# Kernel tuning notes

Measured on AMD Instinct MI355X. Metric: run time of the kernel, lower is better.

The kernel has to match this reference:

```python
import jax, jax.numpy as jnp
import numpy as np

V = 28   # len(string.ascii_lowercase + ' #')
D = 32   # embed dim
H = 2    # heads
DH = D // H
B = 64
S = 1024


def _pe(seq_len, d):
    pos = np.arange(seq_len, dtype=np.float32)[:, None]
    div = np.exp(np.arange(0, d, 2, dtype=np.float32) * (-np.log(10000.0) / d))
    pe = np.zeros((seq_len, d), np.float32)
    pe[:, 0::2] = np.sin(pos * div)
    pe[:, 1::2] = np.cos(pos * div)
    return jnp.asarray(pe)


def setup_inputs() -> dict:
    key = jax.random.key(0)
    ks = jax.random.split(key, 12)
    x = jax.random.randint(ks[0], (B, S), 0, V)
    # per-row valid length in [1, S-4] so last 1-index + 3 stays in range (as original assumes)
    lengths = jax.random.randint(ks[1], (B,), 1, S - 3)
    mask = (jnp.arange(S)[None, :] < lengths[:, None]).astype(jnp.float32)[..., None]
    sc = 1.0 / np.sqrt(D)
    emb = jax.random.normal(ks[2], (V, D), jnp.float32)
    wq = jax.random.normal(ks[3], (D, D), jnp.float32) * sc
    wk = jax.random.normal(ks[4], (D, D), jnp.float32) * sc
    wv = jax.random.normal(ks[5], (D, D), jnp.float32) * sc
    bq = jnp.zeros((D,), jnp.float32)
    bk = jnp.zeros((D,), jnp.float32)
    bv = jnp.zeros((D,), jnp.float32)
    wo = jax.random.normal(ks[6], (D, D), jnp.float32) * sc
    bo = jnp.zeros((D,), jnp.float32)
    w_fc = jax.random.normal(ks[7], (V, D), jnp.float32) * sc
    b_fc = jnp.zeros((V,), jnp.float32)
    pe = _pe(S, D)
    return {"x": x, "mask": mask, "emb": emb, "pe": pe,
            "wq": wq, "bq": bq, "wk": wk, "bk": bk, "wv": wv, "bv": bv,
            "wo": wo, "bo": bo, "w_fc": w_fc, "b_fc": b_fc}


def reference(x, mask, emb, pe, wq, bq, wk, bk, wv, bv, wo, bo, w_fc, b_fc):
    Bn, Sn = x.shape
    h = emb[x] + pe[:Sn]                      # [B,S,D]
    m = mask[..., 0]                          # [B,S]
    # vectorized "last valid index" (replaces per-row python loop + .item())
    valid = m > 0
    last = Sn - 1 - jnp.argmax(valid[:, ::-1], axis=1)   # [B]
    pos = jnp.arange(Sn)
    ext = (pos[None, :] > last[:, None]) & (pos[None, :] <= last[:, None] + 3) \
          & (last[:, None] < Sn - 1)
    nm = jnp.where(ext, jnp.float32(1.0), m)  # extended mask [B,S]
    h = h * nm[..., None]
    # multihead self-attention (torch MultiheadAttention, batch_first)
    def heads(t):
        return t.reshape(Bn, Sn, H, DH).transpose(0, 2, 1, 3)  # [B,H,S,DH]
    q = heads(h @ wq.T + bq)
    k = heads(h @ wk.T + bk)
    v = heads(h @ wv.T + bv)
    scores = jnp.einsum('bhqd,bhkd->bhqk', q, k) / jnp.sqrt(jnp.float32(DH))
    scores = jnp.where((nm == 0)[:, None, None, :], jnp.float32(-1e9), scores)
    a = jax.nn.softmax(scores, axis=-1)
    o = jnp.einsum('bhqk,bhkd->bhqd', a, v).transpose(0, 2, 1, 3).reshape(Bn, Sn, D)
    o = o @ wo.T + bo
    return o @ w_fc.T + b_fc                  # [B,S,V]
```

## Files before the change

### kernel.cpp

```cpp
#include <hip/hip_runtime.h>
#include <math.h>

#define BB 64
#define SS 1024
#define DD 32
#define HH 2
#define DHH 16
#define VV 28
#define QSC 0.3606737602222409f

typedef __attribute__((ext_vector_type(8))) short bf16x8;
typedef __attribute__((ext_vector_type(4))) float f32x4;

__device__ __forceinline__ unsigned pack_hi2(float a, float b) {
    return __builtin_amdgcn_perm(__float_as_uint(b), __float_as_uint(a), 0x07060302u);
}
__device__ __forceinline__ float trunc_hi(float a) {
    return __uint_as_float(__float_as_uint(a) & 0xFFFF0000u);
}
__device__ __forceinline__ unsigned bf_rtne_u(float x) {
    unsigned u = __float_as_uint(x);
    return (u + 0x7FFFu + ((u >> 16) & 1u)) >> 16;
}
__device__ __forceinline__ unsigned pack_rtne2(float a, float b) {
    return bf_rtne_u(a) | (bf_rtne_u(b) << 16);
}
__device__ __forceinline__ bf16x8 as_bf16x8(uint4 u) {
    union { uint4 u; bf16x8 v; } cv; cv.u = u; return cv.v;
}


__global__ __launch_bounds__(256) void k_pre(
        const int* __restrict__ x, const float* __restrict__ mask,
        const float* __restrict__ emb, const float* __restrict__ pe,
        const float* __restrict__ wq, const float* __restrict__ bq,
        const float* __restrict__ wk, const float* __restrict__ bk,
        const float* __restrict__ wv, const float* __restrict__ bv,
        const float* __restrict__ wo, const float* __restrict__ bo,
        const float* __restrict__ wfc, const float* __restrict__ bfc,
        int* __restrict__ e, float* __restrict__ W2, float* __restrict__ b2,
        char* __restrict__ qf, char* __restrict__ kf, char* __restrict__ vf) {
    int bid = blockIdx.x;
    int tid = threadIdx.x;
    if (bid < 1024) {
        __shared__ __align__(16) char hbuf[10240];
        __shared__ __align__(16) float Cb[4][16 * 17];
        char* hHi = hbuf;
        char* hLo = hbuf + 5120;
        int wave = tid >> 6, lane = tid & 63;
        int c = lane & 15, kq = lane >> 4;
        {
            int tt = tid >> 2, q4 = tid & 3;
            int idx = bid * 64 + tt;
            int b = idx >> 10, s = idx & 1023;
            float nm = (mask[b * SS + (s >= 3 ? s - 3 : 0)] != 0.0f) ? 1.0f : 0.0f;
            int tok = x[idx];
            float h[8];
#pragma unroll
            for (int i = 0; i < 8; i++)
                h[i] = (emb[tok * DD + q4 * 8 + i] + pe[s * DD + q4 * 8 + i]) * nm;
            unsigned wh[4], wl[4];
#pragma unroll
            for (int wd = 0; wd < 4; wd++) {
                float a0 = h[2 * wd], a1 = h[2 * wd + 1];
                wh[wd] = pack_hi2(a0, a1);
                wl[wd] = pack_hi2(a0 - trunc_hi(a0), a1 - trunc_hi(a1));
            }
            *(uint4*)(hHi + tt * 80 + q4 * 16) = uint4{wh[0], wh[1], wh[2], wh[3]};
            *(uint4*)(hLo + tt * 80 + q4 * 16) = uint4{wl[0], wl[1], wl[2], wl[3]};
        }
        __syncthreads();
        bf16x8 aHh, aHl;
        {
            int off = (wave * 16 + c) * 80 + kq * 16;
            aHh = *(const bf16x8*)(hHi + off);
            aHl = *(const bf16x8*)(hLo + off);
        }
        int blk_b = bid >> 4;
        int s_w = ((bid * 64) & 1023) + wave * 16;
        const f32x4 z4 = {0.0f, 0.0f, 0.0f, 0.0f};
#pragma unroll
        for (int M = 0; M < 3; M++) {
            const float* W    = M == 0 ? wq : (M == 1 ? wk : wv);
            const float* bias = M == 0 ? bq : (M == 1 ? bk : bv);
            bf16x8 Bh[2], Bl[2];
            float bv_[2];
#pragma unroll
            for (int nt = 0; nt < 2; nt++) {
                const float* wrow = W + (nt * 16 + c) * DD + kq * 8;
                float4 wa = ((const float4*)wrow)[0];
                float4 wb = ((const float4*)wrow)[1];
                float f[8] = {wa.x, wa.y, wa.z, wa.w, wb.x, wb.y, wb.z, wb.w};
                unsigned uh[4], ul[4];
#pragma unroll
                for (int wd = 0; wd < 4; wd++) {
                    float a0 = f[2 * wd], a1 = f[2 * wd + 1];
                    uh[wd] = pack_hi2(a0, a1);
                    ul[wd] = pack_hi2(a0 - trunc_hi(a0), a1 - trunc_hi(a1));
                }
                Bh[nt] = as_bf16x8(uint4{uh[0], uh[1], uh[2], uh[3]});
                Bl[nt] = as_bf16x8(uint4{ul[0], ul[1], ul[2], ul[3]});
                bv_[nt] = bias[nt * 16 + c];
            }
#pragma unroll
            for (int nt = 0; nt < 2; nt++) {
                f32x4 acc = __builtin_amdgcn_mfma_f32_16x16x32_bf16(aHh, Bh[nt], z4, 0, 0, 0);
                acc = __builtin_amdgcn_mfma_f32_16x16x32_bf16(aHl, Bh[nt], acc, 0, 0, 0);
                acc = __builtin_amdgcn_mfma_f32_16x16x32_bf16(aHh, Bl[nt], acc, 0, 0, 0);
#pragma unroll
                for (int r = 0; r < 4; r++) {
                    float val = acc[r] + bv_[nt];
                    if (M == 0) val *= QSC;
                    Cb[wave][(kq * 4 + r) * 17 + c] = val;
                }
                int bh = blk_b * 2 + nt;
                if (M == 0) {
                    int tile = s_w >> 4;
                    int qd = lane >> 4, cc = lane & 15;
                    float f[8];
#pragma unroll
                    for (int j = 0; j < 8; j++) f[j] = Cb[wave][cc * 17 + (qd & 1) * 8 + j];
                    unsigned u[4];
                    if (qd < 2) {
#pragma unroll
                        for (int wd = 0; wd < 4; wd++) u[wd] = pack_hi2(f[2 * wd], f[2 * wd + 1]);
                    } else {
#pragma unroll
                        for (int wd = 0; wd < 4; wd++) {
                            float a0 = f[2 * wd] - trunc_hi(f[2 * wd]);
                            float a1 = f[2 * wd + 1] - trunc_hi(f[2 * wd + 1]);
                            u[wd] = pack_hi2(a0, a1);
                        }
                    }
                    *(uint4*)(qf + ((size_t)((bh << 6) + tile) << 10) + lane * 16)
                        = uint4{u[0], u[1], u[2], u[3]};
                } else if (M == 1) {
                    int cl = lane & 3, qd = (lane >> 2) & 3, t = lane >> 4;
                    int ch = s_w >> 7, g = (s_w >> 6) & 1, c0 = (s_w & 63) >> 2;
                    int keyl = 4 * cl + t;
                    float f[8];
#pragma unroll
                    for (int j = 0; j < 8; j++) f[j] = Cb[wave][keyl * 17 + (qd & 1) * 8 + j];
                    unsigned uh[4];
#pragma unroll
                    for (int wd = 0; wd < 4; wd++) uh[wd] = pack_rtne2(f[2 * wd], f[2 * wd + 1]);
                    char* base = kf + ((size_t)((bh << 3) + ch) << 13)
                               + ((g << 2) + t) * 1024 + qd * 256 + (c0 + cl) * 16;
                    *(uint4*)(base) = uint4{uh[0], uh[1], uh[2], uh[3]};
                } else if (lane < 32) {
                    int ch = s_w >> 7, g = (s_w >> 6) & 1, sub = (s_w >> 5) & 1;
                    int qs = (s_w & 31) >> 3;
                    int qrel = lane >> 4, dh = lane & 15;
                    unsigned u[4];
#pragma unroll
                    for (int wd = 0; wd < 4; wd++) {
                        float f0 = Cb[wave][(qrel * 8 + 2 * wd) * 17 + dh];
                        float f1 = Cb[wave][(qrel * 8 + 2 * wd + 1) * 17 + dh];
                        u[wd] = pack_rtne2(f0, f1);
                    }
                    *(uint4*)(vf + ((size_t)((bh << 3) + ch) << 12)
                              + (g * 2 + sub) * 1024 + (qs + qrel) * 256 + dh * 16)
                        = uint4{u[0], u[1], u[2], u[3]};
                }
            }
        }
    } else if (bid < 1088) {
        int b = bid - 1024;
        int lm = -1;
        for (int s = tid; s < SS; s += 256)
            if (mask[b * SS + s] != 0.0f) lm = s;
        __shared__ int red[256];
        red[tid] = lm;
        __syncthreads();
        for (int off = 128; off > 0; off >>= 1) {
            if (tid < off) red[tid] = max(red[tid], red[tid + off]);
            __syncthreads();
        }
        if (tid == 0) {
            int last = red[0];
            int ee = last;
            if (last < SS - 1) ee = min(last + 3, SS - 1);
            e[b] = ee;
        }
    } else {
        for (int t2 = tid; t2 < VV * DD + VV; t2 += 256) {
            if (t2 < VV * DD) {
                int vv = t2 / DD, i = t2 % DD;
                float a = 0.0f;
                for (int j = 0; j < DD; j++) a += wfc[vv * DD + j] * wo[j * DD + i];
                W2[t2] = a;
            } else {
                int vv = t2 - VV * DD;
                float a = bfc[vv];
                for (int j = 0; j < DD; j++) a += wfc[vv * DD + j] * bo[j];
                b2[vv] = a;
            }
        }
    }
}

__global__ __launch_bounds__(256) void k_attn_fc(
        const char* __restrict__ qf, const char* __restrict__ kf,
        const char* __restrict__ vf, const int* __restrict__ e,
        const float* __restrict__ W2, const float* __restrict__ b2,
        float* __restrict__ out) {
    __shared__ __align__(16) char Pb[18432];
    __shared__ __align__(16) float Ob[32 * 36];
    __shared__ __align__(16) float sW[VV * 36];
    __shared__ float sb[VV];
    int tid = threadIdx.x;
    int qt = blockIdx.x, b = blockIdx.y;

    for (int i = tid; i < VV * DD; i += 256) sW[(i >> 5) * 36 + (i & 31)] = W2[i];
    if (tid < VV) sb[tid] = b2[tid];

    int kmax = e[b] + 1;
    int ng = (kmax + 63) >> 6;

    int wave = tid >> 6, lane = tid & 63, quad = lane >> 4, c = lane & 15;
    int h = wave & 1;
    int ts = wave >> 1;
    int tile = (qt << 1) + ts;
    int bh = b * 2 + h;

    char* Pw = Pb + wave * 4608;
    const char* kbase = kf + ((size_t)(bh << 3) << 13);
    const char* vbase = vf + ((size_t)(bh << 3) << 12);

    bf16x8 aQ = *(const bf16x8*)(qf + ((size_t)((bh << 6) + tile) << 10) + lane * 16);
    const f32x4 z4 = {0.0f, 0.0f, 0.0f, 0.0f};
    f32x4 accO = z4;
    float l_[4] = {0.0f, 0.0f, 0.0f, 0.0f};

#pragma unroll
    for (int g = 0; g < 16; g++) {
        if (g < ng) {
            const char* kg = kbase + (size_t)g * 4096;
            const char* vg = vbase + (size_t)g * 2048;
            bf16x8 bv0 = *(const bf16x8*)(vg + lane * 16);
            bf16x8 bv1 = *(const bf16x8*)(vg + 1024 + lane * 16);
            f32x4 st[4];
#pragma unroll
            for (int t = 0; t < 4; t++) {
                bf16x8 bkh = *(const bf16x8*)(kg + t * 1024 + lane * 16);
                st[t] = __builtin_amdgcn_mfma_f32_16x16x32_bf16(aQ, bkh, z4, 0, 0, 0);
            }
            if (((g + 1) << 6) > kmax) {
#pragma unroll
                for (int t = 0; t < 4; t++) {
                    int key = (g << 6) + 4 * c + t;
                    if (key >= kmax) st[t] = f32x4{-3e38f, -3e38f, -3e38f, -3e38f};
                }
            }
            float p[4][4];
#pragma unroll
            for (int t = 0; t < 4; t++)
#pragma unroll
                for (int r = 0; r < 4; r++) p[t][r] = exp2f(st[t][r]);
            char* Pg = Pw + (g & 1) * 2304;
#pragma unroll
            for (int r = 0; r < 4; r++) {
                l_[r] += (p[0][r] + p[1][r]) + (p[2][r] + p[3][r]);
                unsigned lo = pack_hi2(p[0][r], p[1][r]);
                unsigned hi = pack_hi2(p[2][r], p[3][r]);
                *(uint2*)(Pg + (quad * 4 + r) * 144 + c * 8) = uint2{lo, hi};
            }
            const char* Pra = Pg + c * 144 + quad * 16;
            bf16x8 aP0 = *(const bf16x8*)(Pra);
            bf16x8 aP1 = *(const bf16x8*)(Pra + 64);
            accO = __builtin_amdgcn_mfma_f32_16x16x32_bf16(aP0, bv0, accO, 0, 0, 0);
            accO = __builtin_amdgcn_mfma_f32_16x16x32_bf16(aP1, bv1, accO, 0, 0, 0);
        }
    }

#pragma unroll
    for (int d = 1; d < 16; d <<= 1) {
#pragma unroll
        for (int r = 0; r < 4; r++) l_[r] += __shfl_xor(l_[r], d, 16);
    }

    float* obr = Ob + (ts * 16 + quad * 4) * 36 + h * 16 + c;
#pragma unroll
    for (int r = 0; r < 4; r++) obr[r * 36] = accO[r] / l_[r];
    __syncthreads();

    int rl = tid >> 3, j = tid & 7;
    if (j < 7) {
        const float* orow = Ob + rl * 36;
        float ov[DD];
#pragma unroll
        for (int i = 0; i < DD; i += 4) {
            float4 t4 = *(const float4*)(orow + i);
            ov[i] = t4.x; ov[i + 1] = t4.y; ov[i + 2] = t4.z; ov[i + 3] = t4.w;
        }
        int v0 = j << 2;
        float res[4];
#pragma unroll
        for (int k = 0; k < 4; k++) {
            int vv = v0 + k;
            float a = sb[vv];
#pragma unroll
            for (int d = 0; d < DD; d += 4) {
                float4 w4 = *(const float4*)(sW + vv * 36 + d);
                a += ov[d] * w4.x + ov[d + 1] * w4.y + ov[d + 2] * w4.z + ov[d + 3] * w4.w;
            }
            res[k] = a;
        }
        int q = (qt << 5) + rl;
        size_t off = ((size_t)((b << 10) + q)) * VV + v0;
        *(float4*)(out + off) = float4{res[0], res[1], res[2], res[3]};
    }
}

extern "C" void kernel_launch(void* const* d_in, const int* in_sizes, int n_in,
                              void* d_out, int out_size, void* d_ws, size_t ws_size,
                              hipStream_t stream) {
    const int*   x    = (const int*)d_in[0];
    const float* mask = (const float*)d_in[1];
    const float* emb  = (const float*)d_in[2];
    const float* pe   = (const float*)d_in[3];
    const float* wq   = (const float*)d_in[4];
    const float* bq   = (const float*)d_in[5];
    const float* wk   = (const float*)d_in[6];
    const float* bk   = (const float*)d_in[7];
    const float* wv   = (const float*)d_in[8];
    const float* bv   = (const float*)d_in[9];
    const float* wo   = (const float*)d_in[10];
    const float* bo   = (const float*)d_in[11];
    const float* wfc  = (const float*)d_in[12];
    const float* bfc  = (const float*)d_in[13];
    float* out = (float*)d_out;

    char* ws = (char*)d_ws;
    int*   e  = (int*)ws;
    float* W2 = (float*)(ws + 256);
    float* b2 = (float*)(ws + 3840);
    char*  qf = ws + 4096;
    char*  kf = qf + (size_t)8388608;
    char*  vf = kf + (size_t)8388608;

    hipLaunchKernelGGL(k_pre, dim3(1089), dim3(256), 0, stream,
                       x, mask, emb, pe, wq, bq, wk, bk, wv, bv, wo, bo, wfc, bfc,
                       e, W2, b2, qf, kf, vf);
    hipLaunchKernelGGL(k_attn_fc, dim3(SS / 32, BB), dim3(256), 0, stream,
                       qf, kf, vf, e, W2, b2, out);
}
```

Measured before the change: 131.8 us.

## Compute transposed scores so P feeds PV MFMA from registers, skip LDS staging

Swaps the operand order of the QK^T MFMA so each lane holds key-major score fragments that can be packed directly into the A operand of the PV MFMA. This removes the per-wave LDS P buffer with its writes and reads, and requires a new V layout in the producer kernel. The row-sum reduction becomes a single scalar per lane followed by cross-lane shuffles. It also replaces the division with rcp and remaps block indices to interleave batches. Risks: a layout mismatch between producer and consumer, and the loss of full unrolling over the fixed 16-group loop.

```diff
diff --git a/kernel.cpp b/kernel.cpp
--- a/kernel.cpp
+++ b/kernel.cpp
@@ -136,7 +136,7 @@
                         = uint4{u[0], u[1], u[2], u[3]};
                 } else if (M == 1) {
                     int cl = lane & 3, qd = (lane >> 2) & 3, t = lane >> 4;
-                    int ch = s_w >> 7, g = (s_w >> 6) & 1, c0 = (s_w & 63) >> 2;
+                    int ch = s_w >> 7, g1 = (s_w >> 6) & 1, c0 = (s_w & 63) >> 2;
                     int keyl = 4 * cl + t;
                     float f[8];
 #pragma unroll
@@ -145,11 +145,10 @@
 #pragma unroll
                     for (int wd = 0; wd < 4; wd++) uh[wd] = pack_rtne2(f[2 * wd], f[2 * wd + 1]);
                     char* base = kf + ((size_t)((bh << 3) + ch) << 13)
-                               + ((g << 2) + t) * 1024 + qd * 256 + (c0 + cl) * 16;
+                               + ((g1 << 2) + t) * 1024 + qd * 256 + (c0 + cl) * 16;
                     *(uint4*)(base) = uint4{uh[0], uh[1], uh[2], uh[3]};
                 } else if (lane < 32) {
-                    int ch = s_w >> 7, g = (s_w >> 6) & 1, sub = (s_w >> 5) & 1;
-                    int qs = (s_w & 31) >> 3;
+                    int gg = (s_w >> 6) & 15, Qs = (s_w >> 4) & 3;
                     int qrel = lane >> 4, dh = lane & 15;
                     unsigned u[4];
 #pragma unroll
@@ -158,8 +157,8 @@
                         float f1 = Cb[wave][(qrel * 8 + 2 * wd + 1) * 17 + dh];
                         u[wd] = pack_rtne2(f0, f1);
                     }
-                    *(uint4*)(vf + ((size_t)((bh << 3) + ch) << 12)
-                              + (g * 2 + sub) * 1024 + (qs + qrel) * 256 + dh * 16)
+                    *(uint4*)(vf + ((size_t)((bh << 5) + (gg << 1) + qrel) << 10)
+                              + (Qs * 16 + dh) * 16)
                         = uint4{u[0], u[1], u[2], u[3]};
                 }
             }
@@ -204,12 +203,13 @@
         const char* __restrict__ vf, const int* __restrict__ e,
         const float* __restrict__ W2, const float* __restrict__ b2,
         float* __restrict__ out) {
-    __shared__ __align__(16) char Pb[18432];
     __shared__ __align__(16) float Ob[32 * 36];
     __shared__ __align__(16) float sW[VV * 36];
     __shared__ float sb[VV];
     int tid = threadIdx.x;
-    int qt = blockIdx.x, b = blockIdx.y;
+    int f = blockIdx.x + (blockIdx.y << 5);
+    int b = ((f & 7) << 3) + ((f >> 3) & 7);
+    int qt = f >> 6;
 
     for (int i = tid; i < VV * DD; i += 256) sW[(i >> 5) * 36 + (i & 31)] = W2[i];
     if (tid < VV) sb[tid] = b2[tid];
@@ -218,70 +218,62 @@
     int ng = (kmax + 63) >> 6;
 
     int wave = tid >> 6, lane = tid & 63, quad = lane >> 4, c = lane & 15;
-    int h = wave & 1;
-    int ts = wave >> 1;
+    int h = wave & 1, ts = wave >> 1;
     int tile = (qt << 1) + ts;
     int bh = b * 2 + h;
 
-    char* Pw = Pb + wave * 4608;
     const char* kbase = kf + ((size_t)(bh << 3) << 13);
-    const char* vbase = vf + ((size_t)(bh << 3) << 12);
+    const char* vbase = vf + ((size_t)bh << 15);
 
     bf16x8 aQ = *(const bf16x8*)(qf + ((size_t)((bh << 6) + tile) << 10) + lane * 16);
     const f32x4 z4 = {0.0f, 0.0f, 0.0f, 0.0f};
     f32x4 accO = z4;
-    float l_[4] = {0.0f, 0.0f, 0.0f, 0.0f};
-
-#pragma unroll
-    for (int g = 0; g < 16; g++) {
-        if (g < ng) {
-            const char* kg = kbase + (size_t)g * 4096;
-            const char* vg = vbase + (size_t)g * 2048;
-            bf16x8 bv0 = *(const bf16x8*)(vg + lane * 16);
-            bf16x8 bv1 = *(const bf16x8*)(vg + 1024 + lane * 16);
-            f32x4 st[4];
-#pragma unroll
-            for (int t = 0; t < 4; t++) {
-                bf16x8 bkh = *(const bf16x8*)(kg + t * 1024 + lane * 16);
-                st[t] = __builtin_amdgcn_mfma_f32_16x16x32_bf16(aQ, bkh, z4, 0, 0, 0);
-            }
-            if (((g + 1) << 6) > kmax) {
-#pragma unroll
-                for (int t = 0; t < 4; t++) {
-                    int key = (g << 6) + 4 * c + t;
-                    if (key >= kmax) st[t] = f32x4{-3e38f, -3e38f, -3e38f, -3e38f};
-                }
-            }
-            float p[4][4];
+    float l_ = 0.0f;
+
+    for (int g = 0; g < ng; g++) {
+        const char* kg = kbase + (size_t)g * 4096;
+        const char* vg = vbase + (size_t)g * 2048;
+        bf16x8 bv0 = *(const bf16x8*)(vg + lane * 16);
+        bf16x8 bv1 = *(const bf16x8*)(vg + 1024 + lane * 16);
+        f32x4 st[4];
+#pragma unroll
+        for (int t = 0; t < 4; t++) {
+            bf16x8 aK = *(const bf16x8*)(kg + t * 1024 + lane * 16);
+            st[t] = __builtin_amdgcn_mfma_f32_16x16x32_bf16(aK, aQ, z4, 0, 0, 0);
+        }
+        if (((g + 1) << 6) > kmax) {
+            int kb = (g << 6) + (quad << 4);
 #pragma unroll
             for (int t = 0; t < 4; t++)
 #pragma unroll
-                for (int r = 0; r < 4; r++) p[t][r] = exp2f(st[t][r]);
-            char* Pg = Pw + (g & 1) * 2304;
-#pragma unroll
-            for (int r = 0; r < 4; r++) {
-                l_[r] += (p[0][r] + p[1][r]) + (p[2][r] + p[3][r]);
-                unsigned lo = pack_hi2(p[0][r], p[1][r]);
-                unsigned hi = pack_hi2(p[2][r], p[3][r]);
-                *(uint2*)(Pg + (quad * 4 + r) * 144 + c * 8) = uint2{lo, hi};
-            }
-            const char* Pra = Pg + c * 144 + quad * 16;
-            bf16x8 aP0 = *(const bf16x8*)(Pra);
-            bf16x8 aP1 = *(const bf16x8*)(Pra + 64);
-            accO = __builtin_amdgcn_mfma_f32_16x16x32_bf16(aP0, bv0, accO, 0, 0, 0);
-            accO = __builtin_amdgcn_mfma_f32_16x16x32_bf16(aP1, bv1, accO, 0, 0, 0);
-        }
+                for (int r = 0; r < 4; r++)
+                    if (kb + 4 * r + t >= kmax) st[t][r] = -3e38f;
+        }
+        float p[4][4];
+#pragma unroll
+        for (int t = 0; t < 4; t++)
+#pragma unroll
+            for (int r = 0; r < 4; r++) p[t][r] = exp2f(st[t][r]);
+#pragma unroll
+        for (int t = 0; t < 4; t++)
+            l_ += (p[t][0] + p[t][1]) + (p[t][2] + p[t][3]);
+        bf16x8 pa0 = as_bf16x8(uint4{pack_hi2(p[0][0], p[1][0]), pack_hi2(p[2][0], p[3][0]),
+                                     pack_hi2(p[0][1], p[1][1]), pack_hi2(p[2][1], p[3][1])});
+        bf16x8 pa1 = as_bf16x8(uint4{pack_hi2(p[0][2], p[1][2]), pack_hi2(p[2][2], p[3][2]),
+                                     pack_hi2(p[0][3], p[1][3]), pack_hi2(p[2][3], p[3][3])});
+        accO = __builtin_amdgcn_mfma_f32_16x16x32_bf16(pa0, bv0, accO, 0, 0, 0);
+        accO = __builtin_amdgcn_mfma_f32_16x16x32_bf16(pa1, bv1, accO, 0, 0, 0);
     }
 
-#pragma unroll
-    for (int d = 1; d < 16; d <<= 1) {
-#pragma unroll
-        for (int r = 0; r < 4; r++) l_[r] += __shfl_xor(l_[r], d, 16);
+    l_ += __shfl_xor(l_, 16);
+    l_ += __shfl_xor(l_, 32);
+
+    float* obr = Ob + (ts * 16 + quad * 4) * 36 + h * 16 + c;
+#pragma unroll
+    for (int r = 0; r < 4; r++) {
+        float lr = __shfl(l_, (quad << 2) + r, 16);
+        obr[r * 36] = accO[r] * __builtin_amdgcn_rcpf(lr);
     }
-
-    float* obr = Ob + (ts * 16 + quad * 4) * 36 + h * 16 + c;
-#pragma unroll
-    for (int r = 0; r < 4; r++) obr[r * 36] = accO[r] / l_[r];
     __syncthreads();
 
     int rl = tid >> 3, j = tid & 7;
```

Result: slower. 138.6 us (+5.1%).
